# Kernel optimization log

Measured on AMD Instinct MI355X. Metric: run time of the kernel, lower is better.

The kernel has to match this reference:

```python
import jax, jax.numpy as jnp
import numpy as np

B, T, D, H, L, V = 2, 1024, 1024, 16, 6, 32000
HD = D // H  # head_size = n_emb // n_heads
EPS = 1e-5   # torch LayerNorm default


def setup_inputs() -> dict:
    key = jax.random.key(0)
    ks = jax.random.split(key, 19)
    s = 0.02
    n = lambda k, shape: jax.random.normal(k, shape, dtype=jnp.float32) * s
    return {
        "idx": jax.random.randint(ks[0], (B, T), 0, V),
        "targets": jax.random.randint(ks[1], (B, T), 0, V),
        "tok_emb": n(ks[2], (V, D)),
        "pos_emb": n(ks[3], (V, D)),  # only first T rows used, as in the source
        "Wq": n(ks[4], (L, H, D, HD)),
        "Wk": n(ks[5], (L, H, D, HD)),
        "Wv": n(ks[6], (L, H, D, HD)),
        "Wo": n(ks[7], (L, D, D)),
        "bo": n(ks[8], (L, D)),
        "W1": n(ks[9], (L, D, 4 * D)),
        "b1": n(ks[10], (L, 4 * D)),
        "W2": n(ks[11], (L, 4 * D, D)),
        "b2": n(ks[12], (L, D)),
        "ln_g": jnp.ones((D,), jnp.float32),
        "ln_b": jnp.zeros((D,), jnp.float32),
        "Wf": n(ks[13], (D, V)),
        "bf": n(ks[14], (V,)),
    }


def _layer_norm(x, g, b):
    mu = jnp.mean(x, axis=-1, keepdims=True)
    var = jnp.mean(jnp.square(x - mu), axis=-1, keepdims=True)
    return (x - mu) * jax.lax.rsqrt(var + EPS) * g + b


def _forward(idx, targets, tok_emb, pos_emb, Wq, Wk, Wv, Wo, bo,
             W1, b1, W2, b2, ln_g, ln_b, Wf, bf):
    x = tok_emb[idx] + pos_emb[:T]  # [B,T,D]
    tril = jnp.tril(jnp.ones((T, T), dtype=bool))
    scale = jnp.asarray(D, x.dtype) ** -0.5  # NOTE: source scales by C=N_EMBED, not head_size

    def block(x, p):
        wq, wk, wv, wo, bo_, w1, b1_, w2, b2_ = p
        q = jnp.einsum('btd,hde->bhte', x, wq)
        k = jnp.einsum('btd,hde->bhte', x, wk)
        v = jnp.einsum('btd,hde->bhte', x, wv)
        scores = jnp.einsum('bhte,bhse->bhts', q, k) * scale
        scores = jnp.where(tril, scores, -jnp.inf)
        att = jax.nn.softmax(scores, axis=-1)
        o = jnp.einsum('bhts,bhse->bhte', att, v)
        o = o.transpose(0, 2, 1, 3).reshape(B, T, D)  # concat heads
        x = x + o @ wo + bo_                           # attn residual (no LN in source)
        h = jax.nn.relu(x @ w1 + b1_)
        x = x + h @ w2 + b2_                           # ffn residual
        return x, None

    x, _ = jax.lax.scan(block, x, (Wq, Wk, Wv, Wo, bo, W1, b1, W2, b2))
    x = _layer_norm(x, ln_g, ln_b)
    logits = x @ Wf + bf  # [B,T,V]
    logp = jax.nn.log_softmax(logits, axis=-1)
    nll = -jnp.take_along_axis(logp, targets[..., None], axis=-1)
    loss = jnp.mean(nll)
    return logits, loss


def reference(idx, targets, tok_emb, pos_emb, Wq, Wk, Wv, Wo, bo,
              W1, b1, W2, b2, ln_g, ln_b, Wf, bf):
    return _forward(idx, targets, tok_emb, pos_emb, Wq, Wk, Wv, Wo, bo,
                    W1, b1, W2, b2, ln_g, ln_b, Wf, bf)
```

## Files before the change

kernel.cpp:

```cpp
#include <hip/hip_runtime.h>
#include <hip/hip_bf16.h>

typedef unsigned short u16;
typedef unsigned int u32;
typedef float f32x4 __attribute__((ext_vector_type(4)));
typedef __bf16 bf16x8 __attribute__((ext_vector_type(8)));

#define NB 2
#define NT 1024
#define ND 1024
#define NH 16
#define HDIM 64
#define NL 6
#define NV 32000
#define ND4 4096
#define BT (NB * NT)
#define L2E 1.44269504f
#define NSLOT 500

__device__ __forceinline__ u16 f2b(float f) {
  u32 u = __builtin_bit_cast(u32, f);
  u32 r = (u + 0x7FFFu + ((u >> 16) & 1u)) >> 16;
  return (u16)r;
}

__device__ __forceinline__ void gl_lds16(const void* g, void* lds) {
  __builtin_amdgcn_global_load_lds((const __attribute__((address_space(1))) u32*)g,
                                   (__attribute__((address_space(3))) u32*)lds, 16, 0, 0);
}

__device__ __forceinline__ float rmax16(float v) {
  v = fmaxf(v, __shfl_xor(v, 1, 64));
  v = fmaxf(v, __shfl_xor(v, 2, 64));
  v = fmaxf(v, __shfl_xor(v, 4, 64));
  v = fmaxf(v, __shfl_xor(v, 8, 64));
  return v;
}
__device__ __forceinline__ float rsum16(float v) {
  v += __shfl_xor(v, 1, 64);
  v += __shfl_xor(v, 2, 64);
  v += __shfl_xor(v, 4, 64);
  v += __shfl_xor(v, 8, 64);
  return v;
}

__global__ void k_embed(const int* __restrict__ idx, const float* __restrict__ tok,
                        const float* __restrict__ pos, float* __restrict__ xf,
                        u16* __restrict__ xb) {
  int row = blockIdx.x;
  int t = row & (NT - 1);
  int tk = idx[row];
  int c = threadIdx.x * 4;
  float4 a = *(const float4*)(tok + (size_t)tk * ND + c);
  float4 p = *(const float4*)(pos + (size_t)t * ND + c);
  float4 s = make_float4(a.x + p.x, a.y + p.y, a.z + p.z, a.w + p.w);
  *(float4*)(xf + (size_t)row * ND + c) = s;
  u16* o = xb + (size_t)row * ND + c;
  *(u32*)(o + 0) = (u32)f2b(s.x) | ((u32)f2b(s.y) << 16);
  *(u32*)(o + 2) = (u32)f2b(s.z) | ((u32)f2b(s.w) << 16);
}

__device__ __forceinline__ void tr_tile(const float* in, int in_rs, u16* out, int out_rs,
                                        int k0, int n0, float (*t)[65]) {
  int tid = threadIdx.x;
#pragma unroll
  for (int i = 0; i < 16; ++i) {
    int e = tid + 256 * i;
    int r = e >> 6, c = e & 63;
    t[r][c] = in[(size_t)(k0 + r) * in_rs + n0 + c];
  }
  __syncthreads();
#pragma unroll
  for (int i = 0; i < 16; ++i) {
    int e = tid + 256 * i;
    int r = e >> 6, c = e & 63;
    out[(size_t)(n0 + r) * out_rs + k0 + c] = f2b(t[c][r]);
  }
}

__global__ void k_transpose(const float* __restrict__ in, u16* __restrict__ out,
                            int K, int N) {
  __shared__ float t[64][65];
  tr_tile(in, N, out, K, blockIdx.y * 64, blockIdx.x * 64, t);
}

__global__ void k_trans_layer(const float* __restrict__ Wq, const float* __restrict__ Wk,
                              const float* __restrict__ Wv, const float* __restrict__ Wo,
                              const float* __restrict__ W1, const float* __restrict__ W2,
                              u16* __restrict__ wqkvT, u16* __restrict__ woT,
                              u16* __restrict__ w1T, u16* __restrict__ w2T, int l) {
  __shared__ float t[64][65];
  int i = blockIdx.x;
  if (i < 768) {
    int x = i & 15, z = i >> 4;
    int s = z >> 4, h = z & 15;
    const float* in = (s == 0 ? Wq : s == 1 ? Wk : Wv) + ((size_t)(l * NH + h)) * ND * HDIM;
    u16* o = wqkvT + ((size_t)(s * ND + h * HDIM)) * ND;
    tr_tile(in, HDIM, o, ND, x * 64, 0, t);
  } else if (i < 1024) {
    int j = i - 768, x = j & 15, y = j >> 4;
    tr_tile(Wo + (size_t)l * ND * ND, ND, woT, ND, y * 64, x * 64, t);
  } else if (i < 2048) {
    int j = i - 1024, x = j & 63, y = j >> 6;
    tr_tile(W1 + (size_t)l * ND * ND4, ND4, w1T, ND, y * 64, x * 64, t);
  } else {
    int j = i - 2048, x = j & 15, y = j >> 4;
    tr_tile(W2 + (size_t)l * ND4 * ND, ND, w2T, ND4, y * 64, x * 64, t);
  }
}

template <int EPI>
__global__ void __launch_bounds__(512, 2)
k_gemm8(const u16* __restrict__ A, const u16* __restrict__ Bt,
        const float* __restrict__ bias, float* __restrict__ outf,
        u16* __restrict__ outb, int K, int N, int nMt, float* __restrict__ pl) {
  __shared__ u16 lds[2][2][2][128 * 64];
  int tid = threadIdx.x;
  int w = tid >> 6, l = tid & 63;
  int l4 = l >> 4, lm = l & 15;
  int wm = w >> 2, wn = w & 3;

  int nwg = gridDim.x, bid = blockIdx.x;
  int q8 = nwg >> 3, r8 = nwg & 7;
  int xcd = bid & 7, loc = bid >> 3;
  int swz = (xcd < r8 ? xcd * (q8 + 1) : r8 * (q8 + 1) + (xcd - r8) * q8) + loc;
  int m0 = (swz % nMt) * 256;
  int n0 = (swz / nMt) * 256;

  f32x4 acc[8][4];
  f32x4 z = {0.f, 0.f, 0.f, 0.f};
#pragma unroll
  for (int m = 0; m < 8; ++m)
#pragma unroll
    for (int n = 0; n < 4; ++n) acc[m][n] = z;

  int srow = (w << 3) + (l >> 3);
  int scol = (((l & 7) ^ ((l >> 3) & 7)) << 3);
  int sdst = w * 512 + l * 8;

  auto stage_half = [&](int b, int mat, int h, int kt) {
    int k0 = kt << 6;
    const u16* base = (mat == 0 ? A + (size_t)(m0 + (h << 7)) * K
                                : Bt + (size_t)(n0 + (h << 7)) * K);
#pragma unroll
    for (int i = 0; i < 2; ++i)
      gl_lds16(base + (size_t)(i * 64 + srow) * K + k0 + scol,
               &lds[b][mat][h][i * 4096 + sdst]);
  };

  int c0 = (l4 ^ (lm & 7)) * 8;
  int c1 = c0 ^ 32;
  int brow0 = (wn & 1) * 64;

  const u16* A0h = &lds[0][0][wm][0];
  const u16* B0h = &lds[0][1][wn >> 1][0];
  const u16* A1h = &lds[1][0][wm][0];
  const u16* B1h = &lds[1][1][wn >> 1][0];

  bf16x8 Ar[4][2], Bx[2][2], By[2][2];

  auto dsA = [&](const u16* Ah, int mf0) {
#pragma unroll
    for (int mf = 0; mf < 4; ++mf) {
      Ar[mf][0] = *(const bf16x8*)&Ah[((mf0 + mf) * 16 + lm) * 64 + c0];
      Ar[mf][1] = *(const bf16x8*)&Ah[((mf0 + mf) * 16 + lm) * 64 + c1];
    }
  };
  auto dsB = [&](const u16* Bh, bf16x8 (&B)[2][2], int nf0) {
#pragma unroll
    for (int nf = 0; nf < 2; ++nf) {
      B[nf][0] = *(const bf16x8*)&Bh[(brow0 + (nf0 + nf) * 16 + lm) * 64 + c0];
      B[nf][1] = *(const bf16x8*)&Bh[(brow0 + (nf0 + nf) * 16 + lm) * 64 + c1];
    }
  };
  auto mm = [&](int am, bf16x8 (&B)[2][2], int an) {
    __builtin_amdgcn_s_setprio(1);
#pragma unroll
    for (int mf = 0; mf < 4; ++mf)
#pragma unroll
      for (int nf = 0; nf < 2; ++nf) {
        acc[am + mf][an + nf] =
            __builtin_amdgcn_mfma_f32_16x16x32_bf16(Ar[mf][0], B[nf][0], acc[am + mf][an + nf], 0, 0, 0);
        acc[am + mf][an + nf] =
            __builtin_amdgcn_mfma_f32_16x16x32_bf16(Ar[mf][1], B[nf][1], acc[am + mf][an + nf], 0, 0, 0);
      }
    __builtin_amdgcn_s_setprio(0);
  };
  auto openbar = [&]() {
    __builtin_amdgcn_sched_barrier(0);
    __builtin_amdgcn_s_barrier();
    __builtin_amdgcn_sched_barrier(0);
  };
  auto midbar = [&]() {
    __builtin_amdgcn_sched_barrier(0);
    __builtin_amdgcn_s_barrier();
    asm volatile("s_waitcnt lgkmcnt(0)" ::: "memory");
    __builtin_amdgcn_sched_barrier(0);
  };

  int nk = K >> 6;
  stage_half(0, 0, 0, 0); stage_half(0, 0, 1, 0);
  stage_half(0, 1, 0, 0); stage_half(0, 1, 1, 0);
  stage_half(1, 0, 0, 1);

  for (int u = 0; u < nk; u += 2) {
    bool s2 = (u + 2 < nk), s3 = (u + 3 < nk);
    asm volatile("s_waitcnt vmcnt(2)" ::: "memory");
    openbar();
    dsA(A0h, 0); dsB(B0h, Bx, 0);
    stage_half(1, 0, 1, u + 1);
    midbar();
    mm(0, Bx, 0);
    openbar();
    dsB(B0h, By, 2);
    stage_half(1, 1, 0, u + 1);
    midbar();
    mm(0, By, 2);
    openbar();
    dsA(A0h, 4);
    stage_half(1, 1, 1, u + 1);
    midbar();
    mm(4, By, 2);
    openbar();
    if (s2) stage_half(0, 0, 0, u + 2);
    midbar();
    mm(4, Bx, 0);
    if (s2) asm volatile("s_waitcnt vmcnt(2)" ::: "memory");
    else    asm volatile("s_waitcnt vmcnt(0)" ::: "memory");
    openbar();
    dsA(A1h, 0); dsB(B1h, Bx, 0);
    if (s2) stage_half(0, 0, 1, u + 2);
    midbar();
    mm(0, Bx, 0);
    openbar();
    dsB(B1h, By, 2);
    if (s2) stage_half(0, 1, 0, u + 2);
    midbar();
    mm(0, By, 2);
    openbar();
    dsA(A1h, 4);
    if (s2) stage_half(0, 1, 1, u + 2);
    midbar();
    mm(4, By, 2);
    openbar();
    if (s3) stage_half(1, 0, 0, u + 3);
    midbar();
    mm(4, Bx, 0);
  }

  if constexpr (EPI == 4) {
    int slot = (n0 >> 6) + wn;
#pragma unroll
    for (int mf = 0; mf < 8; ++mf)
#pragma unroll
      for (int j = 0; j < 4; ++j) {
        int row = m0 + wm * 128 + mf * 16 + l4 * 4 + j;
        float sm = 0.f;
#pragma unroll
        for (int nf = 0; nf < 4; ++nf) {
          int col = n0 + wn * 64 + nf * 16 + lm;
          float v = acc[mf][nf][j] + bias[col];
          outf[(size_t)row * N + col] = v;
          sm += exp2f(v * L2E);
        }
        sm = rsum16(sm);
        if (lm == 0) pl[(size_t)row * NSLOT + slot] = sm;
      }
  } else {
#pragma unroll
    for (int mf = 0; mf < 8; ++mf)
#pragma unroll
      for (int nf = 0; nf < 4; ++nf)
#pragma unroll
        for (int j = 0; j < 4; ++j) {
          int row = m0 + wm * 128 + mf * 16 + l4 * 4 + j;
          int col = n0 + wn * 64 + nf * 16 + lm;
          float v = acc[mf][nf][j];
          if constexpr (EPI == 0) outb[(size_t)row * N + col] = f2b(v);
          else outf[(size_t)row * N + col] = v + bias[col];
        }
  }
}

template <int EPI, int BN>
__global__ void __launch_bounds__(256, BN == 64 ? 3 : 2)
k_gemm4(const u16* __restrict__ A, const u16* __restrict__ Bt,
        const float* __restrict__ bias, float* __restrict__ outf,
        u16* __restrict__ outb, int K, int N, int nMt) {
  constexpr int NFW = BN / 32;
  constexpr int NH2 = NFW / 2;
  __shared__ u16 As[2][128 * 64];
  __shared__ u16 Bs[2][BN * 64];
  int tid = threadIdx.x;
  int w = tid >> 6, l = tid & 63;
  int l4 = l >> 4, lm = l & 15;
  int wr = w >> 1, wc = w & 1;

  int nwg = gridDim.x, bid = blockIdx.x;
  int q8 = nwg >> 3, r8 = nwg & 7;
  int xcd = bid & 7, loc = bid >> 3;
  int swz = (xcd < r8 ? xcd * (q8 + 1) : r8 * (q8 + 1) + (xcd - r8) * q8) + loc;
  int m0 = (swz % nMt) * 128;
  int n0 = (swz / nMt) * BN;

  f32x4 acc[4][NFW];
  f32x4 z = {0.f, 0.f, 0.f, 0.f};
#pragma unroll
  for (int m = 0; m < 4; ++m)
#pragma unroll
    for (int n = 0; n < NFW; ++n) acc[m][n] = z;

  int srow = (w << 3) + (l >> 3);
  int scol = (((l & 7) ^ ((l >> 3) & 7)) << 3);
  int sdst = w * 512 + l * 8;

  const u16* Arow = A + (size_t)m0 * K;
  const u16* Brow = Bt + (size_t)n0 * K;

  auto stage = [&](int b, int kt) {
    int k0 = kt << 6;
#pragma unroll
    for (int i = 0; i < 4; ++i)
      gl_lds16(Arow + (size_t)(i * 32 + srow) * K + k0 + scol, &As[b][i * 2048 + sdst]);
#pragma unroll
    for (int i = 0; i < BN / 32; ++i)
      gl_lds16(Brow + (size_t)(i * 32 + srow) * K + k0 + scol, &Bs[b][i * 2048 + sdst]);
  };

  int c0 = (l4 ^ (lm & 7)) * 8;
  int c1 = c0 ^ 32;

  int nk = K >> 6;
  stage(0, 0);
  for (int t = 0; t < nk; ++t) {
    int b = t & 1;
    asm volatile("s_waitcnt vmcnt(0)" ::: "memory");
    __builtin_amdgcn_sched_barrier(0);
    __builtin_amdgcn_s_barrier();
    __builtin_amdgcn_sched_barrier(0);
    if (t + 1 < nk) stage(b ^ 1, t + 1);
    __builtin_amdgcn_sched_barrier(0);

    bf16x8 af[4][2], bfr[NH2][2];
#pragma unroll
    for (int mf = 0; mf < 4; ++mf) {
      af[mf][0] = *(const bf16x8*)&As[b][(mf * 16 + lm) * 64 + c0 + (wr * 64 * 64)];
      af[mf][1] = *(const bf16x8*)&As[b][(mf * 16 + lm) * 64 + c1 + (wr * 64 * 64)];
    }
#pragma unroll
    for (int nf = 0; nf < NH2; ++nf) {
      int brow = wc * (BN / 2) + nf * 16 + lm;
      bfr[nf][0] = *(const bf16x8*)&Bs[b][brow * 64 + c0];
      bfr[nf][1] = *(const bf16x8*)&Bs[b][brow * 64 + c1];
    }
    __builtin_amdgcn_s_setprio(1);
#pragma unroll
    for (int mf = 0; mf < 4; ++mf)
#pragma unroll
      for (int nf = 0; nf < NH2; ++nf) {
        acc[mf][nf] = __builtin_amdgcn_mfma_f32_16x16x32_bf16(af[mf][0], bfr[nf][0], acc[mf][nf], 0, 0, 0);
        acc[mf][nf] = __builtin_amdgcn_mfma_f32_16x16x32_bf16(af[mf][1], bfr[nf][1], acc[mf][nf], 0, 0, 0);
      }
    __builtin_amdgcn_s_setprio(0);

#pragma unroll
    for (int nf = 0; nf < NH2; ++nf) {
      int brow = wc * (BN / 2) + (nf + NH2) * 16 + lm;
      bfr[nf][0] = *(const bf16x8*)&Bs[b][brow * 64 + c0];
      bfr[nf][1] = *(const bf16x8*)&Bs[b][brow * 64 + c1];
    }
    __builtin_amdgcn_s_setprio(1);
#pragma unroll
    for (int mf = 0; mf < 4; ++mf)
#pragma unroll
      for (int nf = 0; nf < NH2; ++nf) {
        acc[mf][nf + NH2] = __builtin_amdgcn_mfma_f32_16x16x32_bf16(af[mf][0], bfr[nf][0], acc[mf][nf + NH2], 0, 0, 0);
        acc[mf][nf + NH2] = __builtin_amdgcn_mfma_f32_16x16x32_bf16(af[mf][1], bfr[nf][1], acc[mf][nf + NH2], 0, 0, 0);
      }
    __builtin_amdgcn_s_setprio(0);
  }

#pragma unroll
  for (int mf = 0; mf < 4; ++mf)
#pragma unroll
    for (int nf = 0; nf < NFW; ++nf)
#pragma unroll
      for (int j = 0; j < 4; ++j) {
        int row = m0 + wr * 64 + mf * 16 + l4 * 4 + j;
        int col = n0 + wc * (BN / 2) + nf * 16 + lm;
        float v = acc[mf][nf][j];
        if constexpr (EPI == 0) {
          outb[(size_t)row * N + col] = f2b(v);
        } else if constexpr (EPI == 2) {
          v += bias[col];
          outb[(size_t)row * N + col] = f2b(fmaxf(v, 0.f));
        } else {
          v += bias[col];
          size_t o = (size_t)row * N + col;
          float nx = outf[o] + v;
          outf[o] = nx;
          outb[o] = f2b(nx);
        }
      }
}

__global__ void __launch_bounds__(512) k_attn(const u16* __restrict__ qkv,
                                              u16* __restrict__ ob) {
  int bid = blockIdx.x;
  int qb = bid & 7, h = (bid >> 3) & 15, b = bid >> 7;
  int tid = threadIdx.x;
  int w = tid >> 6, l = tid & 63;
  int l4 = l >> 4, lm = l & 15;

  __shared__ u16 Ks[128][72];
  __shared__ u16 Vt[64][136];
  __shared__ u16 Pw[8][16][136];

  const u16* base = qkv + (size_t)b * NT * 3072 + h * HDIM;

  bf16x8 qf[2];
#pragma unroll
  for (int kk = 0; kk < 2; ++kk) {
    int tq = qb * 128 + w * 16 + lm;
    qf[kk] = *(const bf16x8*)(base + (size_t)tq * 3072 + kk * 32 + l4 * 8);
  }

  int r0 = tid >> 3, e0 = (tid & 7) << 3;

  auto loadT = [&](int kb, bf16x8& k0, bf16x8& k1, bf16x8& v0, bf16x8& v1) {
    const u16* s0 = base + (size_t)(kb * 128 + r0) * 3072;
    const u16* s1 = s0 + (size_t)64 * 3072;
    k0 = *(const bf16x8*)(s0 + 1024 + e0);
    v0 = *(const bf16x8*)(s0 + 2048 + e0);
    k1 = *(const bf16x8*)(s1 + 1024 + e0);
    v1 = *(const bf16x8*)(s1 + 2048 + e0);
  };

  f32x4 z = {0.f, 0.f, 0.f, 0.f};
  f32x4 oacc[4];
  float mrow[4], lrow[4];
#pragma unroll
  for (int n = 0; n < 4; ++n) oacc[n] = z;
#pragma unroll
  for (int j = 0; j < 4; ++j) { mrow[j] = -1e30f; lrow[j] = 0.f; }

  bf16x8 ck0, ck1, cv0, cv1;
  loadT(0, ck0, ck1, cv0, cv1);
  bf16x8 nk0 = ck0, nk1 = ck1, nv0 = cv0, nv1 = cv1;

  for (int kb = 0; kb <= qb; ++kb) {
    __syncthreads();
    {
      *(bf16x8*)&Ks[r0][e0] = ck0;
      *(bf16x8*)&Ks[r0 + 64][e0] = ck1;
      union { bf16x8 v; u16 u[8]; } a, c;
      a.v = cv0; c.v = cv1;
#pragma unroll
      for (int j = 0; j < 8; ++j) {
        Vt[e0 + j][r0] = a.u[j];
        Vt[e0 + j][r0 + 64] = c.u[j];
      }
    }
    if (kb < qb) loadT(kb + 1, nk0, nk1, nv0, nv1);
    __syncthreads();

    f32x4 s[8];
#pragma unroll
    for (int n = 0; n < 8; ++n) s[n] = z;
#pragma unroll
    for (int kk = 0; kk < 2; ++kk)
#pragma unroll
      for (int n = 0; n < 8; ++n) {
        bf16x8 kf = *(const bf16x8*)&Ks[n * 16 + lm][kk * 32 + l4 * 8];
        s[n] = __builtin_amdgcn_mfma_f32_16x16x32_bf16(qf[kk], kf, s[n], 0, 0, 0);
      }

    bool diag = (kb == qb);
#pragma unroll
    for (int j = 0; j < 4; ++j) {
      int rloc = w * 16 + l4 * 4 + j;
      float pv[8];
      float rm = -1e30f;
#pragma unroll
      for (int n = 0; n < 8; ++n) {
        float vv = s[n][j] * 0.03125f;
        if (diag && (n * 16 + lm > rloc)) vv = -1e30f;
        pv[n] = vv;
        rm = fmaxf(rm, vv);
      }
      rm = rmax16(rm);
      float nm = fmaxf(mrow[j], rm);
      float corr = exp2f((mrow[j] - nm) * L2E);
      mrow[j] = nm;
      float rs = 0.f;
#pragma unroll
      for (int n = 0; n < 8; ++n) {
        float p = exp2f((pv[n] - nm) * L2E);
        pv[n] = p;
        rs += p;
      }
      rs = rsum16(rs);
      lrow[j] = lrow[j] * corr + rs;
#pragma unroll
      for (int n = 0; n < 4; ++n) oacc[n][j] *= corr;
      int prow = l4 * 4 + j;
#pragma unroll
      for (int n = 0; n < 8; ++n) Pw[w][prow][n * 16 + lm] = f2b(pv[n]);
    }
    asm volatile("s_waitcnt lgkmcnt(0)" ::: "memory");
    __builtin_amdgcn_sched_barrier(0);

#pragma unroll
    for (int kk = 0; kk < 4; ++kk) {
      bf16x8 pa = *(const bf16x8*)&Pw[w][lm][kk * 32 + l4 * 8];
#pragma unroll
      for (int n = 0; n < 4; ++n) {
        bf16x8 vf = *(const bf16x8*)&Vt[n * 16 + lm][kk * 32 + l4 * 8];
        oacc[n] = __builtin_amdgcn_mfma_f32_16x16x32_bf16(pa, vf, oacc[n], 0, 0, 0);
      }
    }

    ck0 = nk0; ck1 = nk1; cv0 = nv0; cv1 = nv1;
  }

#pragma unroll
  for (int n = 0; n < 4; ++n)
#pragma unroll
    for (int j = 0; j < 4; ++j) {
      int tq = qb * 128 + w * 16 + l4 * 4 + j;
      int col = h * HDIM + n * 16 + lm;
      float v = oacc[n][j] / lrow[j];
      ob[(size_t)(b * NT + tq) * ND + col] = f2b(v);
    }
}

__global__ void k_ln(const float* __restrict__ xf, const float* __restrict__ g,
                     const float* __restrict__ bta, u16* __restrict__ xb) {
  __shared__ float red[4];
  int row = blockIdx.x, tid = threadIdx.x;
  int w = tid >> 6;
  int c = tid * 4;
  float4 x = *(const float4*)(xf + (size_t)row * ND + c);
  float s = x.x + x.y + x.z + x.w;
#pragma unroll
  for (int off = 1; off < 64; off <<= 1) s += __shfl_xor(s, off, 64);
  if ((tid & 63) == 0) red[w] = s;
  __syncthreads();
  float mu = (red[0] + red[1] + red[2] + red[3]) * (1.0f / ND);
  float d0 = x.x - mu, d1 = x.y - mu, d2 = x.z - mu, d3 = x.w - mu;
  float v = d0 * d0 + d1 * d1 + d2 * d2 + d3 * d3;
  __syncthreads();
#pragma unroll
  for (int off = 1; off < 64; off <<= 1) v += __shfl_xor(v, off, 64);
  if ((tid & 63) == 0) red[w] = v;
  __syncthreads();
  float var = (red[0] + red[1] + red[2] + red[3]) * (1.0f / ND);
  float rs = rsqrtf(var + 1e-5f);
  float4 gg = *(const float4*)(g + c);
  float4 bb = *(const float4*)(bta + c);
  u16* o = xb + (size_t)row * ND + c;
  o[0] = f2b(d0 * rs * gg.x + bb.x);
  o[1] = f2b(d1 * rs * gg.y + bb.y);
  o[2] = f2b(d2 * rs * gg.z + bb.z);
  o[3] = f2b(d3 * rs * gg.w + bb.w);
}

__global__ void k_loss_row2(const float* __restrict__ pl, const float* __restrict__ logits,
                            const int* __restrict__ tgt, float* __restrict__ lossbuf) {
  int row = blockIdx.x, l = threadIdx.x;
  const float* pr = pl + (size_t)row * NSLOT;
  float s = 0.f;
  for (int i = l; i < NSLOT; i += 64) s += pr[i];
#pragma unroll
  for (int off = 1; off < 64; off <<= 1) s += __shfl_xor(s, off, 64);
  if (l == 0) lossbuf[row] = logf(s) - logits[(size_t)row * NV + tgt[row]];
}

__global__ void k_loss_final(const float* __restrict__ lossbuf, float* __restrict__ out) {
  __shared__ float red[4];
  int tid = threadIdx.x;
  float s = 0.f;
  for (int i = tid; i < BT; i += 256) s += lossbuf[i];
#pragma unroll
  for (int off = 1; off < 64; off <<= 1) s += __shfl_xor(s, off, 64);
  if ((tid & 63) == 0) red[tid >> 6] = s;
  __syncthreads();
  if (tid == 0) out[0] = (red[0] + red[1] + red[2] + red[3]) * (1.0f / BT);
}

extern "C" void kernel_launch(void* const* d_in, const int* in_sizes, int n_in,
                              void* d_out, int out_size, void* d_ws, size_t ws_size,
                              hipStream_t stream) {
  const int* idx = (const int*)d_in[0];
  const int* tgt = (const int*)d_in[1];
  const float* tok = (const float*)d_in[2];
  const float* pos = (const float*)d_in[3];
  const float* Wq = (const float*)d_in[4];
  const float* Wk = (const float*)d_in[5];
  const float* Wv = (const float*)d_in[6];
  const float* Wo = (const float*)d_in[7];
  const float* bo = (const float*)d_in[8];
  const float* W1 = (const float*)d_in[9];
  const float* b1 = (const float*)d_in[10];
  const float* W2 = (const float*)d_in[11];
  const float* b2 = (const float*)d_in[12];
  const float* lng = (const float*)d_in[13];
  const float* lnb = (const float*)d_in[14];
  const float* Wf = (const float*)d_in[15];
  const float* bfp = (const float*)d_in[16];
  float* logits = (float*)d_out;
  float* lossp = logits + (size_t)BT * NV;

  char* ws = (char*)d_ws;
  u16* wT = (u16*)ws;
  size_t off = 65536000;
  float* xf = (float*)(ws + off); off += (size_t)BT * ND * 4;
  u16* xb = (u16*)(ws + off);     off += (size_t)BT * ND * 2;
  u16* qkv = (u16*)(ws + off);    off += (size_t)BT * 3 * ND * 2;
  u16* obuf = (u16*)(ws + off);   off += (size_t)BT * ND * 2;
  u16* hb = (u16*)(ws + off);     off += (size_t)BT * ND4 * 2;
  float* pl = (float*)(ws + off); off += (size_t)BT * NSLOT * 4;
  float* lossbuf = (float*)(ws + off);

  u16* wqkvT = wT;
  u16* woT = wT + (size_t)3 * ND * ND;
  u16* w1T = woT + (size_t)ND * ND;
  u16* w2T = w1T + (size_t)ND4 * ND;

  k_embed<<<BT, 256, 0, stream>>>(idx, tok, pos, xf, xb);
  for (int l = 0; l < NL; ++l) {
    k_trans_layer<<<3072, 256, 0, stream>>>(Wq, Wk, Wv, Wo, W1, W2,
                                            wqkvT, woT, w1T, w2T, l);
    k_gemm4<0, 128><<<384, 256, 0, stream>>>(xb, wqkvT, nullptr, nullptr, qkv, ND, 3 * ND, 16);
    k_attn<<<256, 512, 0, stream>>>(qkv, obuf);
    k_gemm4<3, 64><<<256, 256, 0, stream>>>(obuf, woT, bo + (size_t)l * ND, xf, xb, ND, ND, 16);
    k_gemm4<2, 128><<<512, 256, 0, stream>>>(xb, w1T, b1 + (size_t)l * ND4, nullptr, hb, ND, ND4, 16);
    k_gemm4<3, 64><<<256, 256, 0, stream>>>(hb, w2T, b2 + (size_t)l * ND, xf, xb, ND4, ND, 16);
  }
  k_transpose<<<dim3(500, 16), 256, 0, stream>>>(Wf, wT, ND, NV);
  k_ln<<<BT, 256, 0, stream>>>(xf, lng, lnb, xb);
  k_gemm8<4><<<1000, 512, 0, stream>>>(xb, wT, bfp, logits, nullptr, ND, NV, 8, pl);
  k_loss_row2<<<BT, 64, 0, stream>>>(pl, logits, tgt, lossbuf);
  k_loss_final<<<1, 256, 0, stream>>>(lossbuf, lossp);
}
```

Measured before the change: 1.302 ms.

## Overlap next-layer weight transposes with attention via merged kernel and double-buffered weights

Merges the per-layer weight transpose into the attention kernel as extra blocks that transpose the next layer's weights (or the final Wf) into a double-buffered workspace. The transpose work can then fill idle CUs alongside the 256 attention blocks, and separate launches go away. Embedding and the layer-0 transpose are fused into one prologue kernel, and logits stores become nontemporal. This costs more workspace and a larger shared-memory footprint for the transpose blocks, and it relies on correct ordering of the buffer ping-pong.

```diff
diff --git a/kernel.cpp b/kernel.cpp
--- a/kernel.cpp
+++ b/kernel.cpp
@@ -44,69 +44,77 @@
   return v;
 }
 
-__global__ void k_embed(const int* __restrict__ idx, const float* __restrict__ tok,
-                        const float* __restrict__ pos, float* __restrict__ xf,
-                        u16* __restrict__ xb) {
-  int row = blockIdx.x;
-  int t = row & (NT - 1);
-  int tk = idx[row];
-  int c = threadIdx.x * 4;
-  float4 a = *(const float4*)(tok + (size_t)tk * ND + c);
-  float4 p = *(const float4*)(pos + (size_t)t * ND + c);
-  float4 s = make_float4(a.x + p.x, a.y + p.y, a.z + p.z, a.w + p.w);
-  *(float4*)(xf + (size_t)row * ND + c) = s;
-  u16* o = xb + (size_t)row * ND + c;
-  *(u32*)(o + 0) = (u32)f2b(s.x) | ((u32)f2b(s.y) << 16);
-  *(u32*)(o + 2) = (u32)f2b(s.z) | ((u32)f2b(s.w) << 16);
-}
-
-__device__ __forceinline__ void tr_tile(const float* in, int in_rs, u16* out, int out_rs,
-                                        int k0, int n0, float (*t)[65]) {
+__device__ __forceinline__ void tr512(const float* in, int in_rs, u16* out, int out_rs,
+                                      int k0, int n0, float (*t)[65]) {
   int tid = threadIdx.x;
 #pragma unroll
-  for (int i = 0; i < 16; ++i) {
-    int e = tid + 256 * i;
+  for (int i = 0; i < 8; ++i) {
+    int e = tid + 512 * i;
     int r = e >> 6, c = e & 63;
     t[r][c] = in[(size_t)(k0 + r) * in_rs + n0 + c];
   }
   __syncthreads();
 #pragma unroll
-  for (int i = 0; i < 16; ++i) {
-    int e = tid + 256 * i;
+  for (int i = 0; i < 8; ++i) {
+    int e = tid + 512 * i;
     int r = e >> 6, c = e & 63;
     out[(size_t)(n0 + r) * out_rs + k0 + c] = f2b(t[c][r]);
   }
 }
 
-__global__ void k_transpose(const float* __restrict__ in, u16* __restrict__ out,
-                            int K, int N) {
-  __shared__ float t[64][65];
-  tr_tile(in, N, out, K, blockIdx.y * 64, blockIdx.x * 64, t);
-}
-
-__global__ void k_trans_layer(const float* __restrict__ Wq, const float* __restrict__ Wk,
-                              const float* __restrict__ Wv, const float* __restrict__ Wo,
-                              const float* __restrict__ W1, const float* __restrict__ W2,
-                              u16* __restrict__ wqkvT, u16* __restrict__ woT,
-                              u16* __restrict__ w1T, u16* __restrict__ w2T, int l) {
-  __shared__ float t[64][65];
-  int i = blockIdx.x;
+__device__ __forceinline__ void trans512_blk(
+    int i, int l, const float* Wq, const float* Wk, const float* Wv,
+    const float* Wo, const float* W1, const float* W2,
+    u16* wqkvT, u16* woT, u16* w1T, u16* w2T, float (*t)[65]) {
   if (i < 768) {
     int x = i & 15, z = i >> 4;
     int s = z >> 4, h = z & 15;
     const float* in = (s == 0 ? Wq : s == 1 ? Wk : Wv) + ((size_t)(l * NH + h)) * ND * HDIM;
     u16* o = wqkvT + ((size_t)(s * ND + h * HDIM)) * ND;
-    tr_tile(in, HDIM, o, ND, x * 64, 0, t);
+    tr512(in, HDIM, o, ND, x * 64, 0, t);
   } else if (i < 1024) {
     int j = i - 768, x = j & 15, y = j >> 4;
-    tr_tile(Wo + (size_t)l * ND * ND, ND, woT, ND, y * 64, x * 64, t);
+    tr512(Wo + (size_t)l * ND * ND, ND, woT, ND, y * 64, x * 64, t);
   } else if (i < 2048) {
     int j = i - 1024, x = j & 63, y = j >> 6;
-    tr_tile(W1 + (size_t)l * ND * ND4, ND4, w1T, ND, y * 64, x * 64, t);
+    tr512(W1 + (size_t)l * ND * ND4, ND4, w1T, ND, y * 64, x * 64, t);
   } else {
     int j = i - 2048, x = j & 15, y = j >> 4;
-    tr_tile(W2 + (size_t)l * ND4 * ND, ND, w2T, ND4, y * 64, x * 64, t);
-  }
+    tr512(W2 + (size_t)l * ND4 * ND, ND, w2T, ND4, y * 64, x * 64, t);
+  }
+}
+
+__global__ void __launch_bounds__(512) k_pre(const int* __restrict__ idx,
+                                             const float* __restrict__ tok,
+                                             const float* __restrict__ pos,
+                                             float* __restrict__ xf, u16* __restrict__ xb,
+                                             const float* __restrict__ Wq,
+                                             const float* __restrict__ Wk,
+                                             const float* __restrict__ Wv,
+                                             const float* __restrict__ Wo,
+                                             const float* __restrict__ W1,
+                                             const float* __restrict__ W2,
+                                             u16* __restrict__ wT0) {
+  __shared__ float t[64][65];
+  int bid = blockIdx.x;
+  if (bid < 1024) {
+    int tid = threadIdx.x;
+    int row = bid * 2 + (tid >> 8);
+    int tt = row & (NT - 1);
+    int tk = idx[row];
+    int c = (tid & 255) * 4;
+    float4 a = *(const float4*)(tok + (size_t)tk * ND + c);
+    float4 p = *(const float4*)(pos + (size_t)tt * ND + c);
+    float4 s = make_float4(a.x + p.x, a.y + p.y, a.z + p.z, a.w + p.w);
+    *(float4*)(xf + (size_t)row * ND + c) = s;
+    u16* o = xb + (size_t)row * ND + c;
+    *(u32*)(o + 0) = (u32)f2b(s.x) | ((u32)f2b(s.y) << 16);
+    *(u32*)(o + 2) = (u32)f2b(s.z) | ((u32)f2b(s.w) << 16);
+    return;
+  }
+  trans512_blk(bid - 1024, 0, Wq, Wk, Wv, Wo, W1, W2,
+               wT0, wT0 + (size_t)3 * ND * ND, wT0 + (size_t)4 * ND * ND,
+               wT0 + (size_t)8 * ND * ND, t);
 }
 
 template <int EPI>
@@ -260,7 +268,7 @@
         for (int nf = 0; nf < 4; ++nf) {
           int col = n0 + wn * 64 + nf * 16 + lm;
           float v = acc[mf][nf][j] + bias[col];
-          outf[(size_t)row * N + col] = v;
+          __builtin_nontemporal_store(v, &outf[(size_t)row * N + col]);
           sm += exp2f(v * L2E);
         }
         sm = rsum16(sm);
@@ -277,7 +285,7 @@
           int col = n0 + wn * 64 + nf * 16 + lm;
           float v = acc[mf][nf][j];
           if constexpr (EPI == 0) outb[(size_t)row * N + col] = f2b(v);
-          else outf[(size_t)row * N + col] = v + bias[col];
+          else __builtin_nontemporal_store(v + bias[col], &outf[(size_t)row * N + col]);
         }
   }
 }
@@ -404,17 +412,35 @@
       }
 }
 
-__global__ void __launch_bounds__(512) k_attn(const u16* __restrict__ qkv,
-                                              u16* __restrict__ ob) {
+__global__ void __launch_bounds__(512) k_attn_mega(
+    const u16* __restrict__ qkv, u16* __restrict__ ob,
+    const float* __restrict__ Wq, const float* __restrict__ Wk,
+    const float* __restrict__ Wv, const float* __restrict__ Wo,
+    const float* __restrict__ W1, const float* __restrict__ W2,
+    const float* __restrict__ Wf, u16* __restrict__ wTnext,
+    u16* __restrict__ wfT, int lNext) {
+  __shared__ char smem[70656];
   int bid = blockIdx.x;
+  if (bid >= 256) {
+    auto t = reinterpret_cast<float(*)[65]>(smem);
+    int i = bid - 256;
+    if (lNext < NL) {
+      trans512_blk(i, lNext, Wq, Wk, Wv, Wo, W1, W2,
+                   wTnext, wTnext + (size_t)3 * ND * ND, wTnext + (size_t)4 * ND * ND,
+                   wTnext + (size_t)8 * ND * ND, t);
+    } else {
+      int x = i % 500, y = i / 500;
+      tr512(Wf, NV, wfT, ND, y * 64, x * 64, t);
+    }
+    return;
+  }
+  u16* Ks = (u16*)smem;
+  u16* Vt = Ks + 128 * 72;
+  u16* Pw = Vt + 64 * 136;
   int qb = bid & 7, h = (bid >> 3) & 15, b = bid >> 7;
   int tid = threadIdx.x;
   int w = tid >> 6, l = tid & 63;
   int l4 = l >> 4, lm = l & 15;
-
-  __shared__ u16 Ks[128][72];
-  __shared__ u16 Vt[64][136];
-  __shared__ u16 Pw[8][16][136];
 
   const u16* base = qkv + (size_t)b * NT * 3072 + h * HDIM;
 
@@ -451,14 +477,14 @@
   for (int kb = 0; kb <= qb; ++kb) {
     __syncthreads();
     {
-      *(bf16x8*)&Ks[r0][e0] = ck0;
-      *(bf16x8*)&Ks[r0 + 64][e0] = ck1;
+      *(bf16x8*)&Ks[r0 * 72 + e0] = ck0;
+      *(bf16x8*)&Ks[(r0 + 64) * 72 + e0] = ck1;
       union { bf16x8 v; u16 u[8]; } a, c;
       a.v = cv0; c.v = cv1;
 #pragma unroll
       for (int j = 0; j < 8; ++j) {
-        Vt[e0 + j][r0] = a.u[j];
-        Vt[e0 + j][r0 + 64] = c.u[j];
+        Vt[(e0 + j) * 136 + r0] = a.u[j];
+        Vt[(e0 + j) * 136 + r0 + 64] = c.u[j];
       }
     }
     if (kb < qb) loadT(kb + 1, nk0, nk1, nv0, nv1);
@@ -471,7 +497,7 @@
     for (int kk = 0; kk < 2; ++kk)
 #pragma unroll
       for (int n = 0; n < 8; ++n) {
-        bf16x8 kf = *(const bf16x8*)&Ks[n * 16 + lm][kk * 32 + l4 * 8];
+        bf16x8 kf = *(const bf16x8*)&Ks[(n * 16 + lm) * 72 + kk * 32 + l4 * 8];
         s[n] = __builtin_amdgcn_mfma_f32_16x16x32_bf16(qf[kk], kf, s[n], 0, 0, 0);
       }
 
@@ -505,17 +531,17 @@
       for (int n = 0; n < 4; ++n) oacc[n][j] *= corr;
       int prow = l4 * 4 + j;
 #pragma unroll
-      for (int n = 0; n < 8; ++n) Pw[w][prow][n * 16 + lm] = f2b(pv[n]);
+      for (int n = 0; n < 8; ++n) Pw[(w * 16 + prow) * 136 + n * 16 + lm] = f2b(pv[n]);
     }
     asm volatile("s_waitcnt lgkmcnt(0)" ::: "memory");
     __builtin_amdgcn_sched_barrier(0);
 
 #pragma unroll
     for (int kk = 0; kk < 4; ++kk) {
-      bf16x8 pa = *(const bf16x8*)&Pw[w][lm][kk * 32 + l4 * 8];
+      bf16x8 pa = *(const bf16x8*)&Pw[(w * 16 + lm) * 136 + kk * 32 + l4 * 8];
 #pragma unroll
       for (int n = 0; n < 4; ++n) {
-        bf16x8 vf = *(const bf16x8*)&Vt[n * 16 + lm][kk * 32 + l4 * 8];
+        bf16x8 vf = *(const bf16x8*)&Vt[(n * 16 + lm) * 136 + kk * 32 + l4 * 8];
         oacc[n] = __builtin_amdgcn_mfma_f32_16x16x32_bf16(pa, vf, oacc[n], 0, 0, 0);
       }
     }
@@ -612,8 +638,10 @@
   float* lossp = logits + (size_t)BT * NV;
 
   char* ws = (char*)d_ws;
-  u16* wT = (u16*)ws;
-  size_t off = 65536000;
+  u16* wT0 = (u16*)ws;
+  u16* wT1 = wT0 + (size_t)12 * ND * ND;
+  u16* wfT = wT1 + (size_t)12 * ND * ND;
+  size_t off = (size_t)24 * ND * ND * 2 + (size_t)NV * ND * 2;
   float* xf = (float*)(ws + off); off += (size_t)BT * ND * 4;
   u16* xb = (u16*)(ws + off);     off += (size_t)BT * ND * 2;
   u16* qkv = (u16*)(ws + off);    off += (size_t)BT * 3 * ND * 2;
@@ -622,24 +650,24 @@
   float* pl = (float*)(ws + off); off += (size_t)BT * NSLOT * 4;
   float* lossbuf = (float*)(ws + off);
 
-  u16* wqkvT = wT;
-  u16* woT = wT + (size_t)3 * ND * ND;
-  u16* w1T = woT + (size_t)ND * ND;
-  u16* w2T = w1T + (size_t)ND4 * ND;
-
-  k_embed<<<BT, 256, 0, stream>>>(idx, tok, pos, xf, xb);
+  k_pre<<<4096, 512, 0, stream>>>(idx, tok, pos, xf, xb, Wq, Wk, Wv, Wo, W1, W2, wT0);
   for (int l = 0; l < NL; ++l) {
-    k_trans_layer<<<3072, 256, 0, stream>>>(Wq, Wk, Wv, Wo, W1, W2,
-                                            wqkvT, woT, w1T, w2T, l);
+    u16* wTl = (l & 1) ? wT1 : wT0;
+    u16* wTn = (l & 1) ? wT0 : wT1;
+    u16* wqkvT = wTl;
+    u16* woT = wTl + (size_t)3 * ND * ND;
+    u16* w1T = wTl + (size_t)4 * ND * ND;
+    u16* w2T = wTl + (size_t)8 * ND * ND;
     k_gemm4<0, 128><<<384, 256, 0, stream>>>(xb, wqkvT, nullptr, nullptr, qkv, ND, 3 * ND, 16);
-    k_attn<<<256, 512, 0, stream>>>(qkv, obuf);
+    int extra = (l + 1 < NL) ? 3072 : 8000;
+    k_attn_mega<<<256 + extra, 512, 0, stream>>>(qkv, obuf, Wq, Wk, Wv, Wo, W1, W2, Wf,
+                                                 wTn, wfT, l + 1);
     k_gemm4<3, 64><<<256, 256, 0, stream>>>(obuf, woT, bo + (size_t)l * ND, xf, xb, ND, ND, 16);
     k_gemm4<2, 128><<<512, 256, 0, stream>>>(xb, w1T, b1 + (size_t)l * ND4, nullptr, hb, ND, ND4, 16);
     k_gemm4<3, 64><<<256, 256, 0, stream>>>(hb, w2T, b2 + (size_t)l * ND, xf, xb, ND4, ND, 16);
   }
-  k_transpose<<<dim3(500, 16), 256, 0, stream>>>(Wf, wT, ND, NV);
   k_ln<<<BT, 256, 0, stream>>>(xf, lng, lnb, xb);
-  k_gemm8<4><<<1000, 512, 0, stream>>>(xb, wT, bfp, logits, nullptr, ND, NV, 8, pl);
+  k_gemm8<4><<<1000, 512, 0, stream>>>(xb, wfT, bfp, logits, nullptr, ND, NV, 8, pl);
   k_loss_row2<<<BT, 64, 0, stream>>>(pl, logits, tgt, lossbuf);
   k_loss_final<<<1, 256, 0, stream>>>(lossbuf, lossp);
 }
```

New measurement: 1.206 ms. 7.3% less time.
